# Kernel optimization log

Measured on AMD Instinct MI355X. Metric: run time of the kernel, lower is better.

## Reference

```python
import jax, jax.numpy as jnp
import numpy as np

HEADS = 8
DIM_HEAD = 64


def setup_inputs() -> dict:
    key = jax.random.key(0)
    ks = jax.random.split(key, 5)
    dim = 512
    dim_inner = HEADS * DIM_HEAD
    return {
        "fmap": jax.random.normal(ks[0], (8, dim, 32, 32), dtype=jnp.float32),
        "gamma": jnp.ones((dim,), dtype=jnp.float32),
        "wq": jax.random.normal(ks[1], (dim_inner, dim), dtype=jnp.float32) * 0.05,
        "wv": jax.random.normal(ks[2], (dim_inner, dim), dtype=jnp.float32) * 0.05,
        "null_kv": jax.random.normal(ks[3], (2, HEADS, DIM_HEAD), dtype=jnp.float32),
        "wo": jax.random.normal(ks[4], (dim, dim_inner), dtype=jnp.float32) * 0.05,
    }


def reference(fmap, gamma, wq, wv, null_kv, wo):
    b, c, H, W = fmap.shape
    h, d = HEADS, DIM_HEAD
    n = H * W
    scale = d ** (-0.5)

    # ChannelRMSNorm: F.normalize over channel dim * sqrt(dim) * gamma
    l2 = jnp.sqrt(jnp.sum(fmap * fmap, axis=1, keepdims=True))
    x = fmap / jnp.maximum(l2, 1e-12) * (c ** 0.5) * gamma[None, :, None, None]

    # 1x1 convs as channel matmuls -> [b, h, n, d]
    def proj(w):
        t = jnp.einsum('bcxy,oc->boxy', x, w)          # [b, h*d, H, W]
        return t.reshape(b, h, d, n).transpose(0, 1, 3, 2)  # [b, h, n, d]

    q = proj(wq)
    v = proj(wv)
    k = q  # dot_product=False -> to_k is None, k = q

    # prepend null kv token
    nk = jnp.broadcast_to(null_kv[0][None, :, None, :], (b, h, 1, d))
    nv = jnp.broadcast_to(null_kv[1][None, :, None, :], (b, h, 1, d))
    k = jnp.concatenate([nk, k], axis=2)  # [b, h, n+1, d]
    v = jnp.concatenate([nv, v], axis=2)

    # negative squared L2 distance score: -(|q|^2 + |k|^2 - 2 q.k)
    q_sq = jnp.sum(q * q, axis=-1)  # [b, h, n]
    k_sq = jnp.sum(k * k, axis=-1)  # [b, h, n+1]
    qk = jnp.einsum('bhid,bhjd->bhij', q, k)
    sim = -(q_sq[..., :, None] + k_sq[..., None, :] - 2.0 * qk) * scale

    attn = jax.nn.softmax(sim, axis=-1)
    out = jnp.einsum('bhij,bhjd->bhid', attn, v)  # [b, h, n, d]

    out = out.transpose(0, 1, 3, 2).reshape(b, h * d, H, W)
    return jnp.einsum('boxy,co->bcxy', out, wo)
```

## Files before the change

### kernel.cpp

```cpp
#include <hip/hip_runtime.h>
#include <hip/hip_bf16.h>

#define DEV static __device__ __forceinline__

typedef __bf16 bf16x8 __attribute__((ext_vector_type(8)));
typedef float f32x4 __attribute__((ext_vector_type(4)));
typedef float f32x16 __attribute__((ext_vector_type(16)));
typedef unsigned u32x4 __attribute__((ext_vector_type(4)));
typedef unsigned short u16x8 __attribute__((ext_vector_type(8)));
typedef unsigned short u16x4 __attribute__((ext_vector_type(4)));

DEV unsigned short f2bf(float f) {
  unsigned u = __builtin_bit_cast(unsigned, f);
  u += 0x7fffu + ((u >> 16) & 1u);
  return (unsigned short)(u >> 16);
}
DEV float bf2f(unsigned short s) {
  return __builtin_bit_cast(float, (unsigned)s << 16);
}
DEV f32x4 mfma16(bf16x8 a, bf16x8 b, f32x4 c) {
  return __builtin_amdgcn_mfma_f32_16x16x32_bf16(a, b, c, 0, 0, 0);
}
DEV f32x16 mfma32(bf16x8 a, bf16x8 b, f32x16 c) {
  return __builtin_amdgcn_mfma_f32_32x32x16_bf16(a, b, c, 0, 0, 0);
}
DEV bf16x8 ld8(const unsigned short* p) {
  return __builtin_bit_cast(bf16x8, *(const u16x8*)p);
}

__global__ __launch_bounds__(256) void rnorm_k(const float* __restrict__ fmap,
                                               float* __restrict__ rn) {
  int tid = threadIdx.x;
  int nl = tid & 63, cq = tid >> 6;
  int b = blockIdx.y;
  int n = blockIdx.x * 64 + nl;
  const float* p = fmap + ((size_t)(b * 512 + cq * 128)) * 1024 + n;
  float s = 0.f;
#pragma unroll 8
  for (int i = 0; i < 128; ++i) { float v = p[i * 1024]; s += v * v; }
  __shared__ float red[4][64];
  red[cq][nl] = s;
  __syncthreads();
  if (tid < 64) {
    float t = red[0][tid] + red[1][tid] + red[2][tid] + red[3][tid];
    rn[b * 1024 + blockIdx.x * 64 + tid] = 22.62741699796952f / fmaxf(sqrtf(t), 1e-12f);
  }
}

__global__ __launch_bounds__(256) void tnorm_k(const float* __restrict__ fmap,
                                               const float* __restrict__ gamma,
                                               const float* __restrict__ rn,
                                               unsigned short* __restrict__ xt) {
  int b = blockIdx.z, c0 = blockIdx.y * 64, n0 = blockIdx.x * 64;
  __shared__ float t[64][65];
  int tx = threadIdx.x, ty = threadIdx.y;
#pragma unroll
  for (int i = 0; i < 16; ++i) {
    int r = ty * 16 + i;
    t[r][tx] = fmap[((size_t)(b * 512 + c0 + r)) * 1024 + n0 + tx];
  }
  __syncthreads();
  float g = gamma[c0 + tx];
#pragma unroll
  for (int i = 0; i < 16; ++i) {
    int r = ty * 16 + i;
    float val = t[tx][r] * rn[b * 1024 + n0 + r] * g;
    xt[((size_t)(b * 1024 + n0 + r)) * 512 + c0 + tx] = f2bf(val);
  }
}

__global__ __launch_bounds__(256) void cvt3_k(const float* __restrict__ wq,
                                              const float* __restrict__ wv,
                                              const float* __restrict__ wo,
                                              unsigned short* __restrict__ wqb,
                                              unsigned short* __restrict__ wvb,
                                              unsigned short* __restrict__ wob) {
  int g = blockIdx.x >> 7;
  int i = (blockIdx.x & 127) * 256 + threadIdx.x;
  const float* src = (g == 0) ? wq : (g == 1) ? wv : wo;
  unsigned short* dst = (g == 0) ? wqb : (g == 1) ? wvb : wob;
  const float4* s = (const float4*)src;
  float4 a = s[i * 2], b = s[i * 2 + 1];
  u16x8 o;
  o[0] = f2bf(a.x); o[1] = f2bf(a.y); o[2] = f2bf(a.z); o[3] = f2bf(a.w);
  o[4] = f2bf(b.x); o[5] = f2bf(b.y); o[6] = f2bf(b.z); o[7] = f2bf(b.w);
  ((u16x8*)dst)[i] = o;
}

__global__ __launch_bounds__(256) void gemm_qv_k(const unsigned short* __restrict__ A,
                                                 const unsigned short* __restrict__ wqb,
                                                 const unsigned short* __restrict__ wvb,
                                                 unsigned short* __restrict__ QF,
                                                 unsigned short* __restrict__ VF) {
  __shared__ unsigned short a_lds[128][72];
  __shared__ unsigned short b_lds[128][72];
  const unsigned short* Bt = blockIdx.z ? wvb : wqb;
  int tid = threadIdx.x, lane = tid & 63, wid = tid >> 6;
  int wr = wid >> 1, wc = wid & 1;
  int m0 = blockIdx.y * 128, n0 = blockIdx.x * 128;
  f32x4 acc[4][4] = {};
  for (int kt = 0; kt < 512; kt += 64) {
#pragma unroll
    for (int it = 0; it < 4; ++it) {
      int chunk = it * 256 + tid;
      int row = chunk >> 3, col = (chunk & 7) * 8;
      *(u16x8*)(&a_lds[row][col]) = *(const u16x8*)(A + (size_t)(m0 + row) * 512 + kt + col);
      *(u16x8*)(&b_lds[row][col]) = *(const u16x8*)(Bt + (size_t)(n0 + row) * 512 + kt + col);
    }
    __syncthreads();
#pragma unroll
    for (int ks = 0; ks < 2; ++ks) {
      bf16x8 af[4], bfr[4];
#pragma unroll
      for (int rt = 0; rt < 4; ++rt)
        af[rt] = __builtin_bit_cast(bf16x8,
            *(const u16x8*)(&a_lds[wr * 64 + rt * 16 + (lane & 15)][ks * 32 + (lane >> 4) * 8]));
#pragma unroll
      for (int ct = 0; ct < 4; ++ct)
        bfr[ct] = __builtin_bit_cast(bf16x8,
            *(const u16x8*)(&b_lds[wc * 64 + ct * 16 + (lane & 15)][ks * 32 + (lane >> 4) * 8]));
#pragma unroll
      for (int rt = 0; rt < 4; ++rt)
#pragma unroll
        for (int ct = 0; ct < 4; ++ct)
          acc[rt][ct] = mfma16(af[rt], bfr[ct], acc[rt][ct]);
    }
    __syncthreads();
  }
  if (blockIdx.z == 0) {
#pragma unroll
    for (int rt = 0; rt < 4; ++rt)
#pragma unroll
      for (int ct = 0; ct < 4; ++ct)
#pragma unroll
        for (int r = 0; r < 4; ++r) {
          int n = m0 + wr * 64 + rt * 16 + (lane >> 4) * 4 + r;
          int o = n0 + wc * 64 + ct * 16 + (lane & 15);
          int b = n >> 10, nl = n & 1023;
          int h = o >> 6, d = o & 63;
          int bh = b * 8 + h;
          size_t idx = (size_t)(bh * 32 + (nl >> 5)) * 2048 + (d >> 4) * 512 + (nl & 31) * 16 + (d & 15);
          QF[idx] = f2bf(acc[rt][ct][r]);
        }
  } else {
#pragma unroll
    for (int rt = 0; rt < 4; ++rt)
#pragma unroll
      for (int ct = 0; ct < 4; ++ct) {
        int nb = m0 + wr * 64 + rt * 16 + (lane >> 4) * 4;
        int o = n0 + wc * 64 + ct * 16 + (lane & 15);
        int b = nb >> 10, j = nb & 1023;
        int h = o >> 6, d = o & 63;
        int bh = b * 8 + h;
        size_t idx = (size_t)(bh * 32 + (j >> 5)) * 2048 + ((j >> 4) & 1) * 1024 + (d >> 5) * 512 +
                     (d & 31) * 16 + (j & 15);
        u16x4 pk;
#pragma unroll
        for (int r = 0; r < 4; ++r) pk[r] = f2bf(acc[rt][ct][r]);
        *(u16x4*)(VF + idx) = pk;
      }
  }
}

__global__ __launch_bounds__(256) void gemm_o_k(const unsigned short* __restrict__ A,
                                                const unsigned short* __restrict__ Bt,
                                                float* __restrict__ Cp) {
  __shared__ unsigned short a_lds[128][72];
  __shared__ unsigned short b_lds[128][72];
  int tid = threadIdx.x, lane = tid & 63, wid = tid >> 6;
  int wr = wid >> 1, wc = wid & 1;
  int m0 = blockIdx.y * 128, n0 = blockIdx.x * 128;
  f32x4 acc[4][4] = {};
  for (int kt = 0; kt < 512; kt += 64) {
#pragma unroll
    for (int it = 0; it < 4; ++it) {
      int chunk = it * 256 + tid;
      int row = chunk >> 3, col = (chunk & 7) * 8;
      *(u16x8*)(&a_lds[row][col]) = *(const u16x8*)(A + (size_t)(m0 + row) * 512 + kt + col);
      *(u16x8*)(&b_lds[row][col]) = *(const u16x8*)(Bt + (size_t)(n0 + row) * 512 + kt + col);
    }
    __syncthreads();
#pragma unroll
    for (int ks = 0; ks < 2; ++ks) {
      bf16x8 af[4], bfr[4];
#pragma unroll
      for (int rt = 0; rt < 4; ++rt)
        af[rt] = __builtin_bit_cast(bf16x8,
            *(const u16x8*)(&a_lds[wr * 64 + rt * 16 + (lane & 15)][ks * 32 + (lane >> 4) * 8]));
#pragma unroll
      for (int ct = 0; ct < 4; ++ct)
        bfr[ct] = __builtin_bit_cast(bf16x8,
            *(const u16x8*)(&b_lds[wc * 64 + ct * 16 + (lane & 15)][ks * 32 + (lane >> 4) * 8]));
#pragma unroll
      for (int rt = 0; rt < 4; ++rt)
#pragma unroll
        for (int ct = 0; ct < 4; ++ct)
          acc[rt][ct] = mfma16(af[rt], bfr[ct], acc[rt][ct]);
    }
    __syncthreads();
  }
  int bb = n0 >> 10;
#pragma unroll
  for (int rt = 0; rt < 4; ++rt)
#pragma unroll
    for (int ct = 0; ct < 4; ++ct)
#pragma unroll
      for (int r = 0; r < 4; ++r) {
        int row = m0 + wr * 64 + rt * 16 + (lane >> 4) * 4 + r;
        int col = (n0 & 1023) + wc * 64 + ct * 16 + (lane & 15);
        Cp[((size_t)(bb * 512 + row)) * 1024 + col] = acc[rt][ct][r];
      }
}

__global__ __launch_bounds__(256) void qsq_k(const unsigned short* __restrict__ QF,
                                             const float* __restrict__ nkv,
                                             float* __restrict__ qsqs,
                                             float* __restrict__ p0g) {
  const float COEF = 0.18033688011112042f;
  int idx = blockIdx.x * 256 + threadIdx.x;
  int bh = idx >> 10, n = idx & 1023;
  int h = bh & 7;
  const unsigned short* base = QF + (size_t)(bh * 32 + (n >> 5)) * 2048 + (n & 31) * 16;
  const float* nk = nkv + h * 64;
  float s = 0.f, dot = 0.f, nks = 0.f;
#pragma unroll
  for (int ks = 0; ks < 4; ++ks) {
    u16x8 v0 = *(const u16x8*)(base + ks * 512);
    u16x8 v1 = *(const u16x8*)(base + ks * 512 + 8);
#pragma unroll
    for (int e = 0; e < 8; ++e) {
      float f0 = bf2f(v0[e]), f1 = bf2f(v1[e]);
      float n0 = nk[ks * 16 + e], n1 = nk[ks * 16 + 8 + e];
      s += f0 * f0 + f1 * f1;
      dot += f0 * n0 + f1 * n1;
      nks += n0 * n0 + n1 * n1;
    }
  }
  qsqs[idx] = s * COEF;
  p0g[idx] = __builtin_amdgcn_exp2f((2.f * dot - nks) * COEF);
}

__global__ __launch_bounds__(256) void attn_k(const unsigned short* __restrict__ QF,
                                              const unsigned short* __restrict__ VF,
                                              const float* __restrict__ qsqs,
                                              const float* __restrict__ p0g,
                                              const float* __restrict__ nkv,
                                              unsigned short* __restrict__ att) {
  const float C2 = 0.36067376022224085f;
  int bid = blockIdx.x;
  int s0 = bid >> 3;
  int bh = ((bid & 7) << 3) | (s0 & 7);
  int qt = s0 >> 3;
  int b = bh >> 3, h = bh & 7;
  int n0 = qt * 128;
  int tid = threadIdx.x, lane = tid & 63, wid = tid >> 6;
  int l31 = lane & 31, hi = lane >> 5;

  __shared__ float p0_l[128];
  __shared__ float nv_l[64];
  __shared__ float dn_l[4][32];

  if (tid < 128) p0_l[tid] = p0g[bh * 1024 + n0 + tid];
  else if (tid < 192) nv_l[tid - 128] = nkv[512 + h * 64 + (tid - 128)];
  __syncthreads();

  bf16x8 qf[4];
  const unsigned short* qfp = QF + (size_t)(bh * 32 + qt * 4 + wid) * 2048 + l31 * 16 + hi * 8;
#pragma unroll
  for (int ks = 0; ks < 4; ++ks)
    qf[ks] = ld8(qfp + ks * 512);

  f32x16 oacc[2];
#pragma unroll
  for (int dh = 0; dh < 2; ++dh)
#pragma unroll
    for (int r = 0; r < 16; ++r) {
      int row = (r & 3) + 8 * (r >> 2) + 4 * hi;
      oacc[dh][r] = p0_l[wid * 32 + row] * nv_l[dh * 32 + l31];
    }

  f32x4 dsum4 = {0.f, 0.f, 0.f, 0.f};
  const unsigned short* kbase = QF + (size_t)bh * 65536 + l31 * 16 + hi * 8;
  const unsigned short* vbase = VF + (size_t)bh * 65536 + l31 * 16 + hi * 8;
  const float* ksb = qsqs + bh * 1024 + 4 * hi;

  bf16x8 kfA[4], kfB[4], vfA[2][2], vfB[2][2];
  f32x4 ksqA[4], ksqB[4];

#define LOADT(S, JT)                                                        \
  {                                                                         \
    const unsigned short* kp_ = kbase + (JT) * 2048;                        \
    kf##S[0] = ld8(kp_);        kf##S[1] = ld8(kp_ + 512);                  \
    kf##S[2] = ld8(kp_ + 1024); kf##S[3] = ld8(kp_ + 1536);                 \
    const unsigned short* vp_ = vbase + (JT) * 2048;                        \
    vf##S[0][0] = ld8(vp_);        vf##S[0][1] = ld8(vp_ + 1024);           \
    vf##S[1][0] = ld8(vp_ + 512);  vf##S[1][1] = ld8(vp_ + 1536);           \
    const float* kq_ = ksb + (JT) * 32;                                     \
    ksq##S[0] = *(const f32x4*)(kq_);      ksq##S[1] = *(const f32x4*)(kq_ + 8);  \
    ksq##S[2] = *(const f32x4*)(kq_ + 16); ksq##S[3] = *(const f32x4*)(kq_ + 24); \
  }

#define COMPT(S)                                                            \
  {                                                                         \
    f32x16 sacc = {};                                                       \
    sacc = mfma32(kf##S[0], qf[0], sacc);                                   \
    sacc = mfma32(kf##S[1], qf[1], sacc);                                   \
    sacc = mfma32(kf##S[2], qf[2], sacc);                                   \
    sacc = mfma32(kf##S[3], qf[3], sacc);                                   \
    float p[16];                                                            \
    _Pragma("unroll")                                                       \
    for (int r = 0; r < 16; ++r) {                                          \
      p[r] = __builtin_amdgcn_exp2f(sacc[r] * C2 - ksq##S[r >> 2][r & 3]);  \
      dsum4[r & 3] += p[r];                                                 \
    }                                                                       \
    unsigned w[4][2];                                                       \
    _Pragma("unroll")                                                       \
    for (int m = 0; m < 4; ++m) {                                           \
      asm("v_cvt_pk_bf16_f32 %0, %1, %2" : "=v"(w[m][0]) : "v"(p[4 * m]), "v"(p[4 * m + 1]));     \
      asm("v_cvt_pk_bf16_f32 %0, %1, %2" : "=v"(w[m][1]) : "v"(p[4 * m + 2]), "v"(p[4 * m + 3])); \
    }                                                                       \
    _Pragma("unroll")                                                       \
    for (int sj = 0; sj < 2; ++sj) {                                        \
      unsigned a0 = w[2 * sj][0], b0 = w[2 * sj + 1][0];                    \
      unsigned a1 = w[2 * sj][1], b1 = w[2 * sj + 1][1];                    \
      asm("v_permlane32_swap_b32 %0, %1" : "+v"(a0), "+v"(b0));             \
      asm("v_permlane32_swap_b32 %0, %1" : "+v"(a1), "+v"(b1));             \
      u32x4 pw; pw[0] = a0; pw[1] = a1; pw[2] = b0; pw[3] = b1;             \
      bf16x8 pa = __builtin_bit_cast(bf16x8, pw);                           \
      oacc[0] = mfma32(pa, vf##S[0][sj], oacc[0]);                          \
      oacc[1] = mfma32(pa, vf##S[1][sj], oacc[1]);                          \
    }                                                                       \
  }

  LOADT(A, 0)
#pragma unroll 1
  for (int s = 0; s < 15; ++s) {
    LOADT(B, 2 * s + 1)
    COMPT(A)
    LOADT(A, 2 * s + 2)
    COMPT(B)
  }
  LOADT(B, 31)
  COMPT(A)
  COMPT(B)

  float dsum = (dsum4[0] + dsum4[1]) + (dsum4[2] + dsum4[3]);
  dsum += __shfl_xor(dsum, 32);
  dsum += p0_l[wid * 32 + l31];
  float rden = 1.0f / dsum;
  if (hi == 0) dn_l[wid][l31] = rden;
  __syncthreads();

#pragma unroll
  for (int dh = 0; dh < 2; ++dh)
#pragma unroll
    for (int r = 0; r < 16; ++r) {
      int row = (r & 3) + 8 * (r >> 2) + 4 * hi;
      float o = oacc[dh][r] * dn_l[wid][row];
      att[((size_t)(b * 1024 + n0 + wid * 32 + row)) * 512 + h * 64 + dh * 32 + l31] = f2bf(o);
    }
}

extern "C" void kernel_launch(void* const* d_in, const int* in_sizes, int n_in,
                              void* d_out, int out_size, void* d_ws, size_t ws_size,
                              hipStream_t stream) {
  const float* fmap = (const float*)d_in[0];
  const float* gamma = (const float*)d_in[1];
  const float* wq = (const float*)d_in[2];
  const float* wv = (const float*)d_in[3];
  const float* nkv = (const float*)d_in[4];
  const float* wo = (const float*)d_in[5];
  float* out = (float*)d_out;

  const size_t M4 = (size_t)8192 * 512;
  unsigned short* x_t = (unsigned short*)d_ws;
  unsigned short* QF  = x_t + M4;
  unsigned short* VF  = QF + M4;
  unsigned short* att = VF + M4;
  unsigned short* wqb = att + M4;
  unsigned short* wvb = wqb + (size_t)512 * 512;
  unsigned short* wob = wvb + (size_t)512 * 512;
  float* rn   = (float*)(wob + (size_t)512 * 512);
  float* qsqs = rn + 8192;
  float* p0g  = qsqs + 65536;

  cvt3_k<<<384, 256, 0, stream>>>(wq, wv, wo, wqb, wvb, wob);
  rnorm_k<<<dim3(16, 8), 256, 0, stream>>>(fmap, rn);
  tnorm_k<<<dim3(16, 8, 8), dim3(64, 4), 0, stream>>>(fmap, gamma, rn, x_t);
  gemm_qv_k<<<dim3(4, 64, 2), 256, 0, stream>>>(x_t, wqb, wvb, QF, VF);
  qsq_k<<<256, 256, 0, stream>>>(QF, nkv, qsqs, p0g);
  attn_k<<<512, 256, 0, stream>>>(QF, VF, qsqs, p0g, nkv, att);
  gemm_o_k<<<dim3(64, 4), 256, 0, stream>>>(wob, att, out);
}
```

Before: 82.15 us.

## Fuse prep kernels, fold q-norm into QV GEMM, split attention keys across waves

Merges the weight conversion and row-norm kernels into one launch. The q-squared and null-key terms are now computed in the QV GEMM epilogue, which removes the separate qsq kernel. The transposed-norm kernel now writes 8 bf16 values per thread as a vector store. The attention kernel doubles its threads so that two wave groups each handle half the key tiles, and their partial outputs are combined through LDS. s_setprio is also added around the MFMA sections. Together these cut launch count and raise attention parallelism, at the cost of extra LDS traffic, an extra barrier and more register/LDS pressure per block.

```diff
diff --git a/kernel.cpp b/kernel.cpp
--- a/kernel.cpp
+++ b/kernel.cpp
@@ -28,22 +28,42 @@
   return __builtin_bit_cast(bf16x8, *(const u16x8*)p);
 }
 
-__global__ __launch_bounds__(256) void rnorm_k(const float* __restrict__ fmap,
-                                               float* __restrict__ rn) {
-  int tid = threadIdx.x;
-  int nl = tid & 63, cq = tid >> 6;
-  int b = blockIdx.y;
-  int n = blockIdx.x * 64 + nl;
-  const float* p = fmap + ((size_t)(b * 512 + cq * 128)) * 1024 + n;
-  float s = 0.f;
+__global__ __launch_bounds__(256) void prep_k(const float* __restrict__ wq,
+                                              const float* __restrict__ wv,
+                                              const float* __restrict__ wo,
+                                              const float* __restrict__ fmap,
+                                              unsigned short* __restrict__ wqb,
+                                              unsigned short* __restrict__ wvb,
+                                              unsigned short* __restrict__ wob,
+                                              float* __restrict__ rn) {
+  __shared__ float red[4][64];
+  int bid = blockIdx.x, tid = threadIdx.x;
+  if (bid < 384) {
+    int g = bid >> 7;
+    int i = (bid & 127) * 256 + tid;
+    const float* src = (g == 0) ? wq : (g == 1) ? wv : wo;
+    unsigned short* dst = (g == 0) ? wqb : (g == 1) ? wvb : wob;
+    const float4* s = (const float4*)src;
+    float4 a = s[i * 2], b = s[i * 2 + 1];
+    u16x8 o;
+    o[0] = f2bf(a.x); o[1] = f2bf(a.y); o[2] = f2bf(a.z); o[3] = f2bf(a.w);
+    o[4] = f2bf(b.x); o[5] = f2bf(b.y); o[6] = f2bf(b.z); o[7] = f2bf(b.w);
+    ((u16x8*)dst)[i] = o;
+  } else {
+    int bb = bid - 384;
+    int x = bb & 15, b = bb >> 4;
+    int nl = tid & 63, cq = tid >> 6;
+    int n = x * 64 + nl;
+    const float* p = fmap + ((size_t)(b * 512 + cq * 128)) * 1024 + n;
+    float s = 0.f;
 #pragma unroll 8
-  for (int i = 0; i < 128; ++i) { float v = p[i * 1024]; s += v * v; }
-  __shared__ float red[4][64];
-  red[cq][nl] = s;
-  __syncthreads();
-  if (tid < 64) {
-    float t = red[0][tid] + red[1][tid] + red[2][tid] + red[3][tid];
-    rn[b * 1024 + blockIdx.x * 64 + tid] = 22.62741699796952f / fmaxf(sqrtf(t), 1e-12f);
+    for (int i = 0; i < 128; ++i) { float v = p[i * 1024]; s += v * v; }
+    red[cq][nl] = s;
+    __syncthreads();
+    if (tid < 64) {
+      float t = red[0][tid] + red[1][tid] + red[2][tid] + red[3][tid];
+      rn[b * 1024 + x * 64 + tid] = 22.62741699796952f / fmaxf(sqrtf(t), 1e-12f);
+    }
   }
 }
 
@@ -53,45 +73,37 @@
                                                unsigned short* __restrict__ xt) {
   int b = blockIdx.z, c0 = blockIdx.y * 64, n0 = blockIdx.x * 64;
   __shared__ float t[64][65];
-  int tx = threadIdx.x, ty = threadIdx.y;
+  __shared__ float rnl[64], gl[64];
+  int tid = threadIdx.x;
+  int tx = tid & 63, ty = tid >> 6;
 #pragma unroll
   for (int i = 0; i < 16; ++i) {
     int r = ty * 16 + i;
     t[r][tx] = fmap[((size_t)(b * 512 + c0 + r)) * 1024 + n0 + tx];
   }
+  if (tid < 64) rnl[tid] = rn[b * 1024 + n0 + tid];
+  else if (tid < 128) gl[tid - 64] = gamma[c0 + tid - 64];
   __syncthreads();
-  float g = gamma[c0 + tx];
-#pragma unroll
-  for (int i = 0; i < 16; ++i) {
-    int r = ty * 16 + i;
-    float val = t[tx][r] * rn[b * 1024 + n0 + r] * g;
-    xt[((size_t)(b * 1024 + n0 + r)) * 512 + c0 + tx] = f2bf(val);
-  }
-}
-
-__global__ __launch_bounds__(256) void cvt3_k(const float* __restrict__ wq,
-                                              const float* __restrict__ wv,
-                                              const float* __restrict__ wo,
-                                              unsigned short* __restrict__ wqb,
-                                              unsigned short* __restrict__ wvb,
-                                              unsigned short* __restrict__ wob) {
-  int g = blockIdx.x >> 7;
-  int i = (blockIdx.x & 127) * 256 + threadIdx.x;
-  const float* src = (g == 0) ? wq : (g == 1) ? wv : wo;
-  unsigned short* dst = (g == 0) ? wqb : (g == 1) ? wvb : wob;
-  const float4* s = (const float4*)src;
-  float4 a = s[i * 2], b = s[i * 2 + 1];
-  u16x8 o;
-  o[0] = f2bf(a.x); o[1] = f2bf(a.y); o[2] = f2bf(a.z); o[3] = f2bf(a.w);
-  o[4] = f2bf(b.x); o[5] = f2bf(b.y); o[6] = f2bf(b.z); o[7] = f2bf(b.w);
-  ((u16x8*)dst)[i] = o;
+#pragma unroll
+  for (int half = 0; half < 2; ++half) {
+    int nl = (tid >> 3) + half * 32;
+    int cb = (tid & 7) * 8;
+    float s = rnl[nl];
+    u16x8 o;
+#pragma unroll
+    for (int e = 0; e < 8; ++e) o[e] = f2bf(t[cb + e][nl] * s * gl[cb + e]);
+    *(u16x8*)(xt + ((size_t)(b * 1024 + n0 + nl)) * 512 + c0 + cb) = o;
+  }
 }
 
 __global__ __launch_bounds__(256) void gemm_qv_k(const unsigned short* __restrict__ A,
                                                  const unsigned short* __restrict__ wqb,
                                                  const unsigned short* __restrict__ wvb,
+                                                 const float* __restrict__ nkv,
                                                  unsigned short* __restrict__ QF,
-                                                 unsigned short* __restrict__ VF) {
+                                                 unsigned short* __restrict__ VF,
+                                                 float* __restrict__ qsqs,
+                                                 float* __restrict__ p0g) {
   __shared__ unsigned short a_lds[128][72];
   __shared__ unsigned short b_lds[128][72];
   const unsigned short* Bt = blockIdx.z ? wvb : wqb;
@@ -128,20 +140,46 @@
     __syncthreads();
   }
   if (blockIdx.z == 0) {
+    const float COEF = 0.18033688011112042f;
+    int head = blockIdx.x * 2 + wc;
+    const float* nk = nkv + head * 64;
+    float nk_own[4], nks = 0.f;
+#pragma unroll
+    for (int ct = 0; ct < 4; ++ct) {
+      nk_own[ct] = nk[ct * 16 + (lane & 15)];
+      nks += nk_own[ct] * nk_own[ct];
+    }
+    nks += __shfl_xor(nks, 1); nks += __shfl_xor(nks, 2);
+    nks += __shfl_xor(nks, 4); nks += __shfl_xor(nks, 8);
 #pragma unroll
     for (int rt = 0; rt < 4; ++rt)
 #pragma unroll
-      for (int ct = 0; ct < 4; ++ct)
-#pragma unroll
-        for (int r = 0; r < 4; ++r) {
-          int n = m0 + wr * 64 + rt * 16 + (lane >> 4) * 4 + r;
-          int o = n0 + wc * 64 + ct * 16 + (lane & 15);
-          int b = n >> 10, nl = n & 1023;
-          int h = o >> 6, d = o & 63;
-          int bh = b * 8 + h;
-          size_t idx = (size_t)(bh * 32 + (nl >> 5)) * 2048 + (d >> 4) * 512 + (nl & 31) * 16 + (d & 15);
-          QF[idx] = f2bf(acc[rt][ct][r]);
+      for (int r = 0; r < 4; ++r) {
+        float qs = 0.f, dot = 0.f;
+        unsigned short qr[4];
+#pragma unroll
+        for (int ct = 0; ct < 4; ++ct) {
+          unsigned short us = f2bf(acc[rt][ct][r]);
+          qr[ct] = us;
+          float v = bf2f(us);
+          qs += v * v;
+          dot += v * nk_own[ct];
         }
+        int n = m0 + wr * 64 + rt * 16 + (lane >> 4) * 4 + r;
+        int bb = n >> 10, nl = n & 1023;
+        int bh = bb * 8 + head;
+        size_t fidx = (size_t)(bh * 32 + (nl >> 5)) * 2048 + (nl & 31) * 16 + (lane & 15);
+#pragma unroll
+        for (int ct = 0; ct < 4; ++ct) QF[fidx + ct * 512] = qr[ct];
+        qs += __shfl_xor(qs, 1); qs += __shfl_xor(qs, 2);
+        qs += __shfl_xor(qs, 4); qs += __shfl_xor(qs, 8);
+        dot += __shfl_xor(dot, 1); dot += __shfl_xor(dot, 2);
+        dot += __shfl_xor(dot, 4); dot += __shfl_xor(dot, 8);
+        if ((lane & 15) == 0) {
+          qsqs[bh * 1024 + nl] = qs * COEF;
+          p0g[bh * 1024 + nl] = __builtin_amdgcn_exp2f((2.f * dot - nks) * COEF);
+        }
+      }
   } else {
 #pragma unroll
     for (int rt = 0; rt < 4; ++rt)
@@ -212,35 +250,7 @@
       }
 }
 
-__global__ __launch_bounds__(256) void qsq_k(const unsigned short* __restrict__ QF,
-                                             const float* __restrict__ nkv,
-                                             float* __restrict__ qsqs,
-                                             float* __restrict__ p0g) {
-  const float COEF = 0.18033688011112042f;
-  int idx = blockIdx.x * 256 + threadIdx.x;
-  int bh = idx >> 10, n = idx & 1023;
-  int h = bh & 7;
-  const unsigned short* base = QF + (size_t)(bh * 32 + (n >> 5)) * 2048 + (n & 31) * 16;
-  const float* nk = nkv + h * 64;
-  float s = 0.f, dot = 0.f, nks = 0.f;
-#pragma unroll
-  for (int ks = 0; ks < 4; ++ks) {
-    u16x8 v0 = *(const u16x8*)(base + ks * 512);
-    u16x8 v1 = *(const u16x8*)(base + ks * 512 + 8);
-#pragma unroll
-    for (int e = 0; e < 8; ++e) {
-      float f0 = bf2f(v0[e]), f1 = bf2f(v1[e]);
-      float n0 = nk[ks * 16 + e], n1 = nk[ks * 16 + 8 + e];
-      s += f0 * f0 + f1 * f1;
-      dot += f0 * n0 + f1 * n1;
-      nks += n0 * n0 + n1 * n1;
-    }
-  }
-  qsqs[idx] = s * COEF;
-  p0g[idx] = __builtin_amdgcn_exp2f((2.f * dot - nks) * COEF);
-}
-
-__global__ __launch_bounds__(256) void attn_k(const unsigned short* __restrict__ QF,
+__global__ __launch_bounds__(512) void attn_k(const unsigned short* __restrict__ QF,
                                               const unsigned short* __restrict__ VF,
                                               const float* __restrict__ qsqs,
                                               const float* __restrict__ p0g,
@@ -254,8 +264,11 @@
   int b = bh >> 3, h = bh & 7;
   int n0 = qt * 128;
   int tid = threadIdx.x, lane = tid & 63, wid = tid >> 6;
+  int wq = wid & 3, jg = wid >> 2;
   int l31 = lane & 31, hi = lane >> 5;
 
+  __shared__ float ob_l[32][4][64];
+  __shared__ float dsb[4][32];
   __shared__ float p0_l[128];
   __shared__ float nv_l[64];
   __shared__ float dn_l[4][32];
@@ -265,7 +278,7 @@
   __syncthreads();
 
   bf16x8 qf[4];
-  const unsigned short* qfp = QF + (size_t)(bh * 32 + qt * 4 + wid) * 2048 + l31 * 16 + hi * 8;
+  const unsigned short* qfp = QF + (size_t)(bh * 32 + qt * 4 + wq) * 2048 + l31 * 16 + hi * 8;
 #pragma unroll
   for (int ks = 0; ks < 4; ++ks)
     qf[ks] = ld8(qfp + ks * 512);
@@ -276,7 +289,7 @@
 #pragma unroll
     for (int r = 0; r < 16; ++r) {
       int row = (r & 3) + 8 * (r >> 2) + 4 * hi;
-      oacc[dh][r] = p0_l[wid * 32 + row] * nv_l[dh * 32 + l31];
+      oacc[dh][r] = (jg == 0) ? p0_l[wq * 32 + row] * nv_l[dh * 32 + l31] : 0.f;
     }
 
   f32x4 dsum4 = {0.f, 0.f, 0.f, 0.f};
@@ -303,10 +316,12 @@
 #define COMPT(S)                                                            \
   {                                                                         \
     f32x16 sacc = {};                                                       \
+    __builtin_amdgcn_s_setprio(1);                                          \
     sacc = mfma32(kf##S[0], qf[0], sacc);                                   \
     sacc = mfma32(kf##S[1], qf[1], sacc);                                   \
     sacc = mfma32(kf##S[2], qf[2], sacc);                                   \
     sacc = mfma32(kf##S[3], qf[3], sacc);                                   \
+    __builtin_amdgcn_s_setprio(0);                                          \
     float p[16];                                                            \
     _Pragma("unroll")                                                       \
     for (int r = 0; r < 16; ++r) {                                          \
@@ -319,6 +334,7 @@
       asm("v_cvt_pk_bf16_f32 %0, %1, %2" : "=v"(w[m][0]) : "v"(p[4 * m]), "v"(p[4 * m + 1]));     \
       asm("v_cvt_pk_bf16_f32 %0, %1, %2" : "=v"(w[m][1]) : "v"(p[4 * m + 2]), "v"(p[4 * m + 3])); \
     }                                                                       \
+    __builtin_amdgcn_s_setprio(1);                                          \
     _Pragma("unroll")                                                       \
     for (int sj = 0; sj < 2; ++sj) {                                        \
       unsigned a0 = w[2 * sj][0], b0 = w[2 * sj + 1][0];                    \
@@ -330,35 +346,56 @@
       oacc[0] = mfma32(pa, vf##S[0][sj], oacc[0]);                          \
       oacc[1] = mfma32(pa, vf##S[1][sj], oacc[1]);                          \
     }                                                                       \
-  }
-
-  LOADT(A, 0)
+    __builtin_amdgcn_s_setprio(0);                                          \
+  }
+
+  int jb = jg * 16;
+  LOADT(A, jb)
 #pragma unroll 1
-  for (int s = 0; s < 15; ++s) {
-    LOADT(B, 2 * s + 1)
+  for (int s = 0; s < 7; ++s) {
+    LOADT(B, jb + 2 * s + 1)
     COMPT(A)
-    LOADT(A, 2 * s + 2)
+    LOADT(A, jb + 2 * s + 2)
     COMPT(B)
   }
-  LOADT(B, 31)
+  LOADT(B, jb + 15)
   COMPT(A)
   COMPT(B)
 
   float dsum = (dsum4[0] + dsum4[1]) + (dsum4[2] + dsum4[3]);
   dsum += __shfl_xor(dsum, 32);
-  dsum += p0_l[wid * 32 + l31];
-  float rden = 1.0f / dsum;
-  if (hi == 0) dn_l[wid][l31] = rden;
+
+  if (jg == 1) {
+#pragma unroll
+    for (int dh = 0; dh < 2; ++dh)
+#pragma unroll
+      for (int r = 0; r < 16; ++r)
+        ob_l[dh * 16 + r][wq][lane] = oacc[dh][r];
+    if (hi == 0) dsb[wq][l31] = dsum;
+  }
   __syncthreads();
-
-#pragma unroll
-  for (int dh = 0; dh < 2; ++dh)
-#pragma unroll
-    for (int r = 0; r < 16; ++r) {
-      int row = (r & 3) + 8 * (r >> 2) + 4 * hi;
-      float o = oacc[dh][r] * dn_l[wid][row];
-      att[((size_t)(b * 1024 + n0 + wid * 32 + row)) * 512 + h * 64 + dh * 32 + l31] = f2bf(o);
-    }
+  if (jg == 0) {
+#pragma unroll
+    for (int dh = 0; dh < 2; ++dh)
+#pragma unroll
+      for (int r = 0; r < 16; ++r)
+        oacc[dh][r] += ob_l[dh * 16 + r][wq][lane];
+    dsum += dsb[wq][l31] + p0_l[wq * 32 + l31];
+    float rden = 1.0f / dsum;
+    if (hi == 0) dn_l[wq][l31] = rden;
+  }
+  __syncthreads();
+
+  if (jg == 0) {
+#pragma unroll
+    for (int dh = 0; dh < 2; ++dh)
+#pragma unroll
+      for (int r = 0; r < 16; ++r) {
+        int row = (r & 3) + 8 * (r >> 2) + 4 * hi;
+        float o = oacc[dh][r] * dn_l[wq][row];
+        att[((size_t)(b * 1024 + n0 + wq * 32 + row)) * 512 + h * 64 + dh * 32 + l31] = f2bf(o);
+      }
+  }
 }
 
 extern "C" void kernel_launch(void* const* d_in, const int* in_sizes, int n_in,
@@ -384,11 +421,9 @@
   float* qsqs = rn + 8192;
   float* p0g  = qsqs + 65536;
 
-  cvt3_k<<<384, 256, 0, stream>>>(wq, wv, wo, wqb, wvb, wob);
-  rnorm_k<<<dim3(16, 8), 256, 0, stream>>>(fmap, rn);
-  tnorm_k<<<dim3(16, 8, 8), dim3(64, 4), 0, stream>>>(fmap, gamma, rn, x_t);
-  gemm_qv_k<<<dim3(4, 64, 2), 256, 0, stream>>>(x_t, wqb, wvb, QF, VF);
-  qsq_k<<<256, 256, 0, stream>>>(QF, nkv, qsqs, p0g);
-  attn_k<<<512, 256, 0, stream>>>(QF, VF, qsqs, p0g, nkv, att);
+  prep_k<<<512, 256, 0, stream>>>(wq, wv, wo, fmap, wqb, wvb, wob, rn);
+  tnorm_k<<<dim3(16, 8, 8), 256, 0, stream>>>(fmap, gamma, rn, x_t);
+  gemm_qv_k<<<dim3(4, 64, 2), 256, 0, stream>>>(x_t, wqb, wvb, nkv, QF, VF, qsqs, p0g);
+  attn_k<<<512, 512, 0, stream>>>(QF, VF, qsqs, p0g, nkv, att);
   gemm_o_k<<<dim3(64, 4), 256, 0, stream>>>(wob, att, out);
 }
```

Result: faster. 76.93 us (-6.4%).
